# Optimization experiments

Measured on AMD Instinct MI355X. Metric: run time of the kernel, lower is better.

## Reference

```python
import jax, jax.numpy as jnp
import numpy as np

B, N = 256, 2000          # clouds, points per cloud
M1, M2 = 100, 5           # fps sample counts (ratio 0.05 twice)
K1, K2 = 20, 20           # neighbors per cluster (= 1/ratio)
R1, R2, R3 = 0.3, 1.0, 2.0
F1, F2, F3 = 5, 25, 45


def _fps(pts, m):
    # iterative farthest point sampling, deterministic start at index 0
    n = pts.shape[0]
    def step(carry, _):
        mind, last = carry
        d = jnp.sum((pts - pts[last]) ** 2, axis=-1)
        mind = jnp.minimum(mind, d)
        return (mind, jnp.argmax(mind).astype(jnp.int32)), last
    _, idx = jax.lax.scan(step, (jnp.full((n,), 1e10, pts.dtype), jnp.int32(0)), None, length=m)
    return idx


def _radius_knn(q, pts, k, r):
    # k nearest neighbors of each query, masked to the radius ball (static-shape gnn.radius)
    d = jnp.sum((q[:, None, :] - pts[None, :, :]) ** 2, axis=-1)  # (M, n)
    negd, idx = jax.lax.top_k(-d, k)
    return idx, (-negd) <= r * r


def _masked_max(h, mask):
    return jnp.max(jnp.where(mask[..., None], h, -1e10), axis=1)


def _forward(points, W1, b1, W2, b2, W3, b3, D1, bD1, D2, bD2, D3, bD3):
    def per_cloud(pts):
        # ---- encode level 1 ----
        samples = pts[_fps(pts, M1)]                              # (M1,3)
        idx1, m1 = _radius_knn(samples, pts, K1, R1)
        rel = (pts[idx1] - samples[:, None, :]) / R1 * m1[..., None]   # (M1,K1,3)
        f1 = _masked_max(jax.nn.relu(rel @ W1 + b1), m1)          # (M1,F1)
        # ---- encode level 2 ----
        samples2 = samples[_fps(samples, M2)]                     # (M2,3)
        idx2, m2 = _radius_knn(samples2, samples, K2, R2)
        rel2 = (samples[idx2] - samples2[:, None, :]) / R2 * m2[..., None]
        h2 = jax.nn.relu(jnp.concatenate([rel2, f1[idx2]], axis=-1) @ W2 + b2)
        f2 = _masked_max(h2, m2)                                  # (M2,F2)
        # ---- encode level 3 (global) ----
        rel3 = samples2 / R3
        h3 = jax.nn.relu(jnp.concatenate([rel3, f2], axis=-1) @ W3 + b3)
        latent = jnp.max(h3, axis=0)                              # (F3,)
        # ---- hierarchical decode ----
        o1 = (latent @ D1 + bD1).reshape(M2, 3 + F2)
        dec, cf = o1[:, :3], jax.nn.relu(o1[:, 3:])               # (M2,3),(M2,F2)
        o2 = (cf @ D2 + bD2).reshape(M2 * K2, 3 + F1)
        dec2, cf2 = o2[:, :3], jax.nn.relu(o2[:, 3:])             # (M2*K2,3/F1)
        dec3 = (cf2 @ D3 + bD3).reshape(M2 * K2 * K1, 3)
        # ---- reconstruction: repeat_interleave + add + scale ----
        s2_out = dec * R3
        s_out = (jnp.repeat(s2_out, K2, axis=0) + dec2) * R2
        return (jnp.repeat(s_out, K1, axis=0) + dec3) * R1        # (N,3)
    return jax.vmap(per_cloud)(points).reshape(B * N, 3)


def setup_inputs():
    key = jax.random.key(0)
    ks = jax.random.split(key, 8)
    p = lambda k, s: jax.random.normal(k, s, jnp.float32) * 0.1
    z = lambda s: jnp.zeros((s,), jnp.float32)
    return {
        "points": jax.random.normal(ks[0], (B, N, 3), jnp.float32),
        "W1": p(ks[1], (3, F1)), "b1": z(F1),
        "W2": p(ks[2], (3 + F1, F2)), "b2": z(F2),
        "W3": p(ks[3], (3 + F2, F3)), "b3": z(F3),
        "D1": p(ks[4], (F3, M2 * (3 + F2))), "bD1": z(M2 * (3 + F2)),
        "D2": p(ks[5], (F2, K2 * (3 + F1))), "bD2": z(K2 * (3 + F1)),
        "D3": p(ks[6], (F1, K1 * 3)), "bD3": z(K1 * 3),
    }


def reference(points, W1, b1, W2, b2, W3, b3, D1, bD1, D2, bD2, D3, bD3):
    return _forward(points, W1, b1, W2, b2, W3, b3, D1, bD1, D2, bD2, D3, bD3)
```

## Files before the change

kernel.cpp:

```cpp
#include <hip/hip_runtime.h>

#define TPB 512
#define NW 8
#define NPTS 2000
#define M1C 100
#define M2C 5
#define KNN 20
#define CANDCAP 128

__device__ __forceinline__ float dist3(float px, float py, float pz,
                                       float qx, float qy, float qz) {
#pragma clang fp contract(off)
    float dx = px - qx, dy = py - qy, dz = pz - qz;
    return dx * dx + dy * dy + dz * dz;
}

#define ARGMAX_STEP(ctrl, rm)                                                        \
    do {                                                                             \
        float ov = __int_as_float(__builtin_amdgcn_update_dpp(                       \
            (int)0xff800000, __float_as_int(v), ctrl, rm, 0xf, false));              \
        int oi = __builtin_amdgcn_update_dpp(0x7fffffff, i, ctrl, rm, 0xf, false);   \
        bool take = (ov > v) || (ov == v && oi < i);                                 \
        v = take ? ov : v;                                                           \
        i = take ? oi : i;                                                           \
    } while (0)

__device__ __forceinline__ void wave_argmax(float& v, int& i) {
    ARGMAX_STEP(0x111, 0xf);
    ARGMAX_STEP(0x112, 0xf);
    ARGMAX_STEP(0x114, 0xf);
    ARGMAX_STEP(0x118, 0xf);
    ARGMAX_STEP(0x142, 0xa);
    ARGMAX_STEP(0x143, 0xc);
    v = __int_as_float(__builtin_amdgcn_readlane(__float_as_int(v), 63));
    i = __builtin_amdgcn_readlane(i, 63);
}

#define FMAX_STEP(ctrl, rm)                                                          \
    do {                                                                             \
        float _t = __int_as_float(__builtin_amdgcn_update_dpp(                       \
            (int)0xff800000, __float_as_int(x), ctrl, rm, 0xf, false));              \
        x = fmaxf(x, _t);                                                            \
    } while (0)

__device__ __forceinline__ float wave_fmax(float x) {
    FMAX_STEP(0x111, 0xf);
    FMAX_STEP(0x112, 0xf);
    FMAX_STEP(0x114, 0xf);
    FMAX_STEP(0x118, 0xf);
    FMAX_STEP(0x142, 0xa);
    FMAX_STEP(0x143, 0xc);
    return __int_as_float(__builtin_amdgcn_readlane(__float_as_int(x), 63));
}

__global__ __launch_bounds__(TPB, 2) void fused_kernel(
    const float* __restrict__ P,
    const float* __restrict__ W1, const float* __restrict__ b1,
    const float* __restrict__ W2, const float* __restrict__ b2,
    const float* __restrict__ W3, const float* __restrict__ b3,
    const float* __restrict__ D1, const float* __restrict__ bD1,
    const float* __restrict__ D2, const float* __restrict__ bD2,
    const float* __restrict__ D3, const float* __restrict__ bD3,
    float* __restrict__ out)
{
    __shared__ float smpx[M1C], smpy[M1C], smpz[M1C];
    __shared__ float s2x[M2C], s2y[M2C], s2z[M2C];
    __shared__ float f1s[M1C][5];
    __shared__ float knd[NW][CANDCAP];
    __shared__ int   kni[NW][CANDCAP];
    __shared__ __align__(16) float4 sA[2][4];
    __shared__ __align__(16) float  sZ[2][4];
    __shared__ int flags[4];
    __shared__ float f2s[M2C][25];
    __shared__ float latent[45];
    __shared__ float decv[M2C][3];
    __shared__ float cfs[M2C][25];
    __shared__ float dec2s[M1C][3];
    __shared__ float cf2s[M1C][5];
    __shared__ float w2s[200], b2s[25], w3s[1260], b3s[45];

    const int b = blockIdx.x;
    const int tid = threadIdx.x;
    const int lane = tid & 63;
    const int wid = tid >> 6;

    const float R1SQ = (float)(0.3 * 0.3);
    const float R2SQ = 1.0f;
    const float INVR1 = 1.0f / 0.3f;

    const float* Pb = P + (size_t)b * (NPTS * 3);

    for (int t = tid; t < 200; t += TPB) w2s[t] = W2[t];
    for (int t = tid; t < 25; t += TPB) b2s[t] = b2[t];
    for (int t = tid; t < 1260; t += TPB) w3s[t] = W3[t];
    for (int t = tid; t < 45; t += TPB) b3s[t] = b3[t];
    if (tid < 4) flags[tid] = 0;
    __syncthreads();

    if (wid < 4) {
        __builtin_amdgcn_s_setprio(3);
        float px[8], py[8], pz[8], mind[8];
#pragma unroll
        for (int k = 0; k < 8; ++k) {
            int j = tid + (k << 8);
            bool v = j < NPTS;
            int jc = v ? j : 0;
            px[k] = v ? Pb[3 * jc + 0] : 1e18f;
            py[k] = v ? Pb[3 * jc + 1] : 1e18f;
            pz[k] = v ? Pb[3 * jc + 2] : 1e18f;
            mind[k] = v ? 1e10f : -1.0f;
        }

        float qx = Pb[0], qy = Pb[1], qz = Pb[2];
        for (int it = 0; it < M1C; ++it) {
            if (tid == 0) { smpx[it] = qx; smpy[it] = qy; smpz[it] = qz; }
            float m[8];
#pragma unroll
            for (int k = 0; k < 8; ++k) {
                float d = dist3(px[k], py[k], pz[k], qx, qy, qz);
                m[k] = fminf(mind[k], d);
                mind[k] = m[k];
            }
            float va = m[0]; int ka = 0; if (m[1] > va) { va = m[1]; ka = 1; }
            float vb = m[2]; int kb = 2; if (m[3] > vb) { vb = m[3]; kb = 3; }
            float vc = m[4]; int kc = 4; if (m[5] > vc) { vc = m[5]; kc = 5; }
            float vd = m[6]; int kd = 6; if (m[7] > vd) { vd = m[7]; kd = 7; }
            if (vb > va) { va = vb; ka = kb; }
            if (vd > vc) { vc = vd; kc = kd; }
            if (vc > va) { va = vc; ka = kc; }
            float bv = va; int bi = tid + (ka << 8);
            if (it == M1C - 1) {
                if (lane == 0)
                    __hip_atomic_store(&flags[wid], M1C, __ATOMIC_RELEASE,
                                       __HIP_MEMORY_SCOPE_WORKGROUP);
                break;
            }
            float lv = bv; int li = bi;
            wave_argmax(bv, bi);
            int p = it & 1;
            if (lv == bv && li == bi) {
                int k = bi >> 8;
                float cx = px[0], cy = py[0], cz = pz[0];
#pragma unroll
                for (int kk = 1; kk < 8; ++kk) {
                    bool t = (k == kk);
                    cx = t ? px[kk] : cx;
                    cy = t ? py[kk] : cy;
                    cz = t ? pz[kk] : cz;
                }
                sA[p][wid] = make_float4(bv, __int_as_float(bi), cx, cy);
                sZ[p][wid] = cz;
            }
            if (lane == 0)
                __hip_atomic_store(&flags[wid], it + 1, __ATOMIC_RELEASE,
                                   __HIP_MEMORY_SCOPE_WORKGROUP);
            for (;;) {
                int f = 0x7fffffff;
                if (lane < 4)
                    f = __hip_atomic_load(&flags[lane], __ATOMIC_ACQUIRE,
                                          __HIP_MEMORY_SCOPE_WORKGROUP);
                if (__ballot(f >= it + 1) == ~0ull) break;
            }
            float4 a0 = sA[p][0], a1 = sA[p][1], a2 = sA[p][2], a3 = sA[p][3];
            float4 z0 = *(const float4*)&sZ[p][0];
            float cv0 = a0.x; int ci0 = __float_as_int(a0.y);
            float x0 = a0.z, y0 = a0.w, zz0 = z0.x;
            {
                int ii = __float_as_int(a1.y);
                bool t = (a1.x > cv0) || (a1.x == cv0 && ii < ci0);
                if (t) { cv0 = a1.x; ci0 = ii; x0 = a1.z; y0 = a1.w; zz0 = z0.y; }
            }
            float cv1 = a2.x; int ci1 = __float_as_int(a2.y);
            float x1 = a2.z, y1 = a2.w, zz1 = z0.z;
            {
                int ii = __float_as_int(a3.y);
                bool t = (a3.x > cv1) || (a3.x == cv1 && ii < ci1);
                if (t) { cv1 = a3.x; ci1 = ii; x1 = a3.z; y1 = a3.w; zz1 = z0.w; }
            }
            bool t = (cv1 > cv0) || (cv1 == cv0 && ci1 < ci0);
            qx = t ? x1 : x0; qy = t ? y1 : y0; qz = t ? zz1 : zz0;
        }

        if (wid == 0) {
            float ax = smpx[lane], ay = smpy[lane], az = smpz[lane];
            bool vb2 = lane < (M1C - 64);
            float bx2 = vb2 ? smpx[lane + 64] : 1e18f;
            float by2 = vb2 ? smpy[lane + 64] : 1e18f;
            float bz2 = vb2 ? smpz[lane + 64] : 1e18f;
            float m2a = 1e10f;
            float m2b = vb2 ? 1e10f : -1.0f;
            int last2 = 0;
            for (int it = 0; it < M2C; ++it) {
                float fx = smpx[last2], fy = smpy[last2], fz = smpz[last2];
                if (lane == 0) { s2x[it] = fx; s2y[it] = fy; s2z[it] = fz; }
                m2a = fminf(m2a, dist3(ax, ay, az, fx, fy, fz));
                m2b = fminf(m2b, dist3(bx2, by2, bz2, fx, fy, fz));
                float v = m2a; int i = lane;
                if (m2b > v) { v = m2b; i = lane + 64; }
                wave_argmax(v, i);
                last2 = i;
            }
        }
        __builtin_amdgcn_s_setprio(0);
    } else {
        __builtin_amdgcn_s_setprio(0);
        float rw1[15], rb1[5];
#pragma unroll
        for (int i = 0; i < 15; ++i) rw1[i] = W1[i];
#pragma unroll
        for (int i = 0; i < 5; ++i) rb1[i] = b1[i];

        for (int s = wid - 4; s < M1C; s += 4) {
            while (__hip_atomic_load(&flags[0], __ATOMIC_ACQUIRE,
                                     __HIP_MEMORY_SCOPE_WORKGROUP) <= s)
                __builtin_amdgcn_s_sleep(2);
            float qx = smpx[s], qy = smpy[s], qz = smpz[s];
            int cn = 0;
#pragma unroll 4
            for (int c = 0; c < 32; ++c) {
                int j = c * 64 + lane;
                float d = 0.0f; bool pred = false;
                if (j < NPTS) {
                    d = dist3(Pb[3 * j], Pb[3 * j + 1], Pb[3 * j + 2], qx, qy, qz);
                    pred = (d <= R1SQ);
                }
                unsigned long long mb = __ballot(pred);
                if (pred) {
                    int pos = cn + (int)__popcll(mb & ((1ull << lane) - 1ull));
                    if (pos < CANDCAP) { knd[wid][pos] = d; kni[wid][pos] = j; }
                }
                cn += (int)__popcll(mb);
            }
            if (cn > CANDCAP) cn = CANDCAP;
            float fmx[5];
#pragma unroll
            for (int f = 0; f < 5; ++f) fmx[f] = -1e30f;
            for (int t = lane; t < cn; t += 64) {
                float d = knd[wid][t]; int j = kni[wid][t];
                bool valid = true;
                if (cn > KNN) {
                    int rank = 0;
                    for (int u = 0; u < cn; ++u) {
                        float du = knd[wid][u]; int iu = kni[wid][u];
                        rank += (du < d || (du == d && iu < j)) ? 1 : 0;
                    }
                    valid = rank < KNN;
                }
                if (valid) {
                    float rx = (Pb[3 * j] - qx) * INVR1;
                    float ry = (Pb[3 * j + 1] - qy) * INVR1;
                    float rz = (Pb[3 * j + 2] - qz) * INVR1;
#pragma unroll
                    for (int f = 0; f < 5; ++f) {
                        float h = fmaf(rx, rw1[f], fmaf(ry, rw1[5 + f], fmaf(rz, rw1[10 + f], rb1[f])));
                        fmx[f] = fmaxf(fmx[f], fmaxf(h, 0.0f));
                    }
                }
            }
#pragma unroll
            for (int f = 0; f < 5; ++f) fmx[f] = wave_fmax(fmx[f]);
            if (lane == 0) {
#pragma unroll
                for (int f = 0; f < 5; ++f) f1s[s][f] = fmx[f];
            }
        }
    }
    __syncthreads();

    for (int s = wid; s < M2C; s += NW) {
        float qx2 = s2x[s], qy2 = s2y[s], qz2 = s2z[s];
        int cn = 0;
#pragma unroll
        for (int c = 0; c < 2; ++c) {
            int j = c * 64 + lane;
            float d = 0.0f; bool pred = false;
            if (j < M1C) {
                d = dist3(smpx[j], smpy[j], smpz[j], qx2, qy2, qz2);
                pred = (d <= R2SQ);
            }
            unsigned long long mb = __ballot(pred);
            if (pred) {
                int pos = cn + (int)__popcll(mb & ((1ull << lane) - 1ull));
                knd[wid][pos] = d; kni[wid][pos] = j;
            }
            cn += (int)__popcll(mb);
        }
        float hmx[25];
#pragma unroll
        for (int f = 0; f < 25; ++f) hmx[f] = -1e30f;
        for (int t = lane; t < cn; t += 64) {
            float d = knd[wid][t]; int j = kni[wid][t];
            bool valid = true;
            if (cn > KNN) {
                int rank = 0;
                for (int u = 0; u < cn; ++u) {
                    float du = knd[wid][u]; int iu = kni[wid][u];
                    rank += (du < d || (du == d && iu < j)) ? 1 : 0;
                }
                valid = rank < KNN;
            }
            if (valid) {
                float in8[8];
                in8[0] = smpx[j] - qx2; in8[1] = smpy[j] - qy2; in8[2] = smpz[j] - qz2;
#pragma unroll
                for (int f = 0; f < 5; ++f) in8[3 + f] = f1s[j][f];
#pragma unroll
                for (int f = 0; f < 25; ++f) {
                    float h = b2s[f];
#pragma unroll
                    for (int i = 0; i < 8; ++i) h = fmaf(in8[i], w2s[i * 25 + f], h);
                    hmx[f] = fmaxf(hmx[f], fmaxf(h, 0.0f));
                }
            }
        }
#pragma unroll
        for (int f = 0; f < 25; ++f) {
            float mx = wave_fmax(hmx[f]);
            if (lane == 0) f2s[s][f] = mx;
        }
    }
    __syncthreads();

    if (wid == 0 && lane < 45) {
        float lm = -1e30f;
        for (int r = 0; r < M2C; ++r) {
            float h = b3s[lane];
            h = fmaf(s2x[r] * 0.5f, w3s[0 * 45 + lane], h);
            h = fmaf(s2y[r] * 0.5f, w3s[1 * 45 + lane], h);
            h = fmaf(s2z[r] * 0.5f, w3s[2 * 45 + lane], h);
#pragma unroll
            for (int i = 0; i < 25; ++i) h = fmaf(f2s[r][i], w3s[(3 + i) * 45 + lane], h);
            lm = fmaxf(lm, fmaxf(h, 0.0f));
        }
        latent[lane] = lm;
    }
    __syncthreads();

    for (int t = tid; t < 140; t += TPB) {
        float acc = bD1[t];
        for (int i = 0; i < 45; i++) acc = fmaf(latent[i], D1[i * 140 + t], acc);
        int r = t / 28, c = t % 28;
        if (c < 3) decv[r][c] = acc;
        else cfs[r][c - 3] = fmaxf(acc, 0.0f);
    }
    __syncthreads();

    for (int t = tid; t < 800; t += TPB) {
        int r = t / 160, c = t % 160;
        float acc = bD2[c];
        for (int i = 0; i < 25; i++) acc = fmaf(cfs[r][i], D2[i * 160 + c], acc);
        int g = r * 20 + c / 8, c8 = c % 8;
        if (c8 < 3) dec2s[g][c8] = acc;
        else cf2s[g][c8 - 3] = fmaxf(acc, 0.0f);
    }
    __syncthreads();

    float* outb = out + (size_t)b * (NPTS * 3);
    for (int t = tid; t < NPTS * 3; t += TPB) {
        int n = t / 3, c = t % 3;
        int g = n / 20;
        int m = n / 400;
        int r60 = (n % 20) * 3 + c;
        float acc = bD3[r60];
        for (int i = 0; i < 5; i++) acc = fmaf(cf2s[g][i], D3[i * 60 + r60], acc);
        float val = ((decv[m][c] * 2.0f + dec2s[g][c]) + acc) * 0.3f;
        outb[t] = val;
    }
}

extern "C" void kernel_launch(void* const* d_in, const int* in_sizes, int n_in,
                              void* d_out, int out_size, void* d_ws, size_t ws_size,
                              hipStream_t stream) {
    const float* P   = (const float*)d_in[0];
    const float* W1  = (const float*)d_in[1];
    const float* b1  = (const float*)d_in[2];
    const float* W2  = (const float*)d_in[3];
    const float* b2  = (const float*)d_in[4];
    const float* W3  = (const float*)d_in[5];
    const float* b3  = (const float*)d_in[6];
    const float* D1  = (const float*)d_in[7];
    const float* bD1 = (const float*)d_in[8];
    const float* D2  = (const float*)d_in[9];
    const float* bD2 = (const float*)d_in[10];
    const float* D3  = (const float*)d_in[11];
    const float* bD3 = (const float*)d_in[12];
    float* out = (float*)d_out;

    int B = in_sizes[0] / (NPTS * 3);
    hipLaunchKernelGGL(fused_kernel, dim3(B), dim3(TPB), 0, stream,
                       P, W1, b1, W2, b2, W3, b3, D1, bD1, D2, bD2, D3, bD3, out);
}
```

Before: 214.6 us.

## Stage cloud points in LDS, drop setprio, and restructure level-2 MLP per feature

Copies each cloud's 2000 points into shared memory (SoA) up front so FPS init and the level-1 radius/KNN passes read LDS instead of strided global loads. Removes the wave priority boosts for the FPS waves and adds s_sleep in the spin-wait. Level-2 MLP now compacts valid neighbor inputs into shared memory and lets 25 lanes each compute one output feature, removing 25 wave-wide max reductions. This adds about 24KB of LDS, which may reduce occupancy, and the sleep may add latency to the FPS critical path.

```diff
diff --git a/kernel.cpp b/kernel.cpp
--- a/kernel.cpp
+++ b/kernel.cpp
@@ -63,11 +63,13 @@
     const float* __restrict__ D3, const float* __restrict__ bD3,
     float* __restrict__ out)
 {
+    __shared__ float sx[NPTS], sy[NPTS], sz[NPTS];
     __shared__ float smpx[M1C], smpy[M1C], smpz[M1C];
     __shared__ float s2x[M2C], s2y[M2C], s2z[M2C];
     __shared__ float f1s[M1C][5];
     __shared__ float knd[NW][CANDCAP];
     __shared__ int   kni[NW][CANDCAP];
+    __shared__ float vin[M2C][KNN][8];
     __shared__ __align__(16) float4 sA[2][4];
     __shared__ __align__(16) float  sZ[2][4];
     __shared__ int flags[4];
@@ -89,7 +91,11 @@
     const float INVR1 = 1.0f / 0.3f;
 
     const float* Pb = P + (size_t)b * (NPTS * 3);
-
+    for (int j = tid; j < NPTS; j += TPB) {
+        sx[j] = Pb[3 * j + 0];
+        sy[j] = Pb[3 * j + 1];
+        sz[j] = Pb[3 * j + 2];
+    }
     for (int t = tid; t < 200; t += TPB) w2s[t] = W2[t];
     for (int t = tid; t < 25; t += TPB) b2s[t] = b2[t];
     for (int t = tid; t < 1260; t += TPB) w3s[t] = W3[t];
@@ -98,20 +104,19 @@
     __syncthreads();
 
     if (wid < 4) {
-        __builtin_amdgcn_s_setprio(3);
         float px[8], py[8], pz[8], mind[8];
 #pragma unroll
         for (int k = 0; k < 8; ++k) {
             int j = tid + (k << 8);
             bool v = j < NPTS;
             int jc = v ? j : 0;
-            px[k] = v ? Pb[3 * jc + 0] : 1e18f;
-            py[k] = v ? Pb[3 * jc + 1] : 1e18f;
-            pz[k] = v ? Pb[3 * jc + 2] : 1e18f;
+            px[k] = v ? sx[jc] : 1e18f;
+            py[k] = v ? sy[jc] : 1e18f;
+            pz[k] = v ? sz[jc] : 1e18f;
             mind[k] = v ? 1e10f : -1.0f;
         }
 
-        float qx = Pb[0], qy = Pb[1], qz = Pb[2];
+        float qx = sx[0], qy = sy[0], qz = sz[0];
         for (int it = 0; it < M1C; ++it) {
             if (tid == 0) { smpx[it] = qx; smpy[it] = qy; smpz[it] = qz; }
             float m[8];
@@ -160,6 +165,7 @@
                     f = __hip_atomic_load(&flags[lane], __ATOMIC_ACQUIRE,
                                           __HIP_MEMORY_SCOPE_WORKGROUP);
                 if (__ballot(f >= it + 1) == ~0ull) break;
+                __builtin_amdgcn_s_sleep(1);
             }
             float4 a0 = sA[p][0], a1 = sA[p][1], a2 = sA[p][2], a3 = sA[p][3];
             float4 z0 = *(const float4*)&sZ[p][0];
@@ -201,9 +207,7 @@
                 last2 = i;
             }
         }
-        __builtin_amdgcn_s_setprio(0);
     } else {
-        __builtin_amdgcn_s_setprio(0);
         float rw1[15], rb1[5];
 #pragma unroll
         for (int i = 0; i < 15; ++i) rw1[i] = W1[i];
@@ -221,7 +225,7 @@
                 int j = c * 64 + lane;
                 float d = 0.0f; bool pred = false;
                 if (j < NPTS) {
-                    d = dist3(Pb[3 * j], Pb[3 * j + 1], Pb[3 * j + 2], qx, qy, qz);
+                    d = dist3(sx[j], sy[j], sz[j], qx, qy, qz);
                     pred = (d <= R1SQ);
                 }
                 unsigned long long mb = __ballot(pred);
@@ -247,9 +251,9 @@
                     valid = rank < KNN;
                 }
                 if (valid) {
-                    float rx = (Pb[3 * j] - qx) * INVR1;
-                    float ry = (Pb[3 * j + 1] - qy) * INVR1;
-                    float rz = (Pb[3 * j + 2] - qz) * INVR1;
+                    float rx = (sx[j] - qx) * INVR1;
+                    float ry = (sy[j] - qy) * INVR1;
+                    float rz = (sz[j] - qz) * INVR1;
 #pragma unroll
                     for (int f = 0; f < 5; ++f) {
                         float h = fmaf(rx, rw1[f], fmaf(ry, rw1[5 + f], fmaf(rz, rw1[10 + f], rb1[f])));
@@ -285,38 +289,46 @@
             }
             cn += (int)__popcll(mb);
         }
-        float hmx[25];
-#pragma unroll
-        for (int f = 0; f < 25; ++f) hmx[f] = -1e30f;
-        for (int t = lane; t < cn; t += 64) {
-            float d = knd[wid][t]; int j = kni[wid][t];
-            bool valid = true;
-            if (cn > KNN) {
-                int rank = 0;
-                for (int u = 0; u < cn; ++u) {
-                    float du = knd[wid][u]; int iu = kni[wid][u];
-                    rank += (du < d || (du == d && iu < j)) ? 1 : 0;
-                }
-                valid = rank < KNN;
-            }
+        int nv = 0;
+#pragma unroll
+        for (int c = 0; c < 2; ++c) {
+            int t = c * 64 + lane;
+            bool valid = false;
+            float in8[8];
+            if (t < cn) {
+                float d = knd[wid][t]; int j = kni[wid][t];
+                valid = true;
+                if (cn > KNN) {
+                    int rank = 0;
+                    for (int u = 0; u < cn; ++u) {
+                        float du = knd[wid][u]; int iu = kni[wid][u];
+                        rank += (du < d || (du == d && iu < j)) ? 1 : 0;
+                    }
+                    valid = rank < KNN;
+                }
+                if (valid) {
+                    in8[0] = smpx[j] - qx2; in8[1] = smpy[j] - qy2; in8[2] = smpz[j] - qz2;
+#pragma unroll
+                    for (int f = 0; f < 5; ++f) in8[3 + f] = f1s[j][f];
+                }
+            }
+            unsigned long long mb = __ballot(valid);
             if (valid) {
-                float in8[8];
-                in8[0] = smpx[j] - qx2; in8[1] = smpy[j] - qy2; in8[2] = smpz[j] - qz2;
-#pragma unroll
-                for (int f = 0; f < 5; ++f) in8[3 + f] = f1s[j][f];
-#pragma unroll
-                for (int f = 0; f < 25; ++f) {
-                    float h = b2s[f];
-#pragma unroll
-                    for (int i = 0; i < 8; ++i) h = fmaf(in8[i], w2s[i * 25 + f], h);
-                    hmx[f] = fmaxf(hmx[f], fmaxf(h, 0.0f));
-                }
-            }
-        }
-#pragma unroll
-        for (int f = 0; f < 25; ++f) {
-            float mx = wave_fmax(hmx[f]);
-            if (lane == 0) f2s[s][f] = mx;
+                int pos = nv + (int)__popcll(mb & ((1ull << lane) - 1ull));
+#pragma unroll
+                for (int i = 0; i < 8; ++i) vin[s][pos][i] = in8[i];
+            }
+            nv += (int)__popcll(mb);
+        }
+        if (lane < 25) {
+            float hmx = -1e30f;
+            for (int c = 0; c < nv; ++c) {
+                float h = b2s[lane];
+#pragma unroll
+                for (int i = 0; i < 8; ++i) h = fmaf(vin[s][c][i], w2s[i * 25 + lane], h);
+                hmx = fmaxf(hmx, fmaxf(h, 0.0f));
+            }
+            f2s[s][lane] = hmx;
         }
     }
     __syncthreads();
```

Measured after the change: 192.7 us. -10.2%, faster.
